# Kernel optimization log

Hardware: AMD Instinct MI355X
Metric: run time of the kernel (lower is better)

The kernel has to match this reference:

```python
import jax, jax.numpy as jnp
import numpy as np

B, N, FD, D, HF, WF = 4, 6, 256, 128, 64, 120
IMG_H, IMG_W = 480, 960
EPS_LN = 1e-5


def bilinear_sample(fmap, pts):
    """fmap: (B,C,H,W); pts: (B,P,2) xy pixel coords. Returns (B,P,C) values
    (zeros padding, align_corners=True convention) and (B,P) in-bounds mask."""
    Bc, C, H, W = fmap.shape
    flat = fmap.reshape(Bc, C, H * W)
    x, y = pts[..., 0], pts[..., 1]
    x0, y0 = jnp.floor(x), jnp.floor(y)
    out = jnp.zeros((Bc, pts.shape[1], C), fmap.dtype)
    for dx in (0.0, 1.0):
        for dy in (0.0, 1.0):
            cx, cy = x0 + dx, y0 + dy
            wgt = (1.0 - jnp.abs(x - cx)) * (1.0 - jnp.abs(y - cy))
            inb = (cx >= 0) & (cx <= W - 1) & (cy >= 0) & (cy <= H - 1)
            idx = (jnp.clip(cy, 0, H - 1) * W + jnp.clip(cx, 0, W - 1)).astype(jnp.int32)
            g = jnp.take_along_axis(flat, idx[:, None, :], axis=2)  # (B,C,P)
            out = out + (g * (wgt * inb)[:, None, :]).transpose(0, 2, 1)
    valid = (x >= 0) & (x <= W - 1) & (y >= 0) & (y <= H - 1)
    return out, valid


def _l2norm(x, axis):
    n = jnp.sqrt(jnp.sum(x * x, axis=axis, keepdims=True))
    return x / jnp.maximum(n, 1e-12)


def _ln(x, g, b):
    mu = jnp.mean(x, axis=-1, keepdims=True)
    var = jnp.mean((x - mu) ** 2, axis=-1, keepdims=True)
    return (x - mu) / jnp.sqrt(var + EPS_LN) * g + b


def setup_inputs() -> dict:
    key = jax.random.key(0)
    ks = jax.random.split(key, 12)
    rng = np.random.RandomState(0)
    feature = jax.random.normal(ks[0], (B, N, FD, HF, WF), jnp.float32)
    # realistic intrinsics (same K family for src/tar so homographies land in-frame)
    K = np.zeros((B, N, 3, 3), np.float32)
    K[..., 0, 0] = IMG_W * 0.8 * (1 + 0.01 * rng.randn(B, N))
    K[..., 1, 1] = IMG_W * 0.8 * (1 + 0.01 * rng.randn(B, N))
    K[..., 0, 2] = IMG_W / 2
    K[..., 1, 2] = IMG_H / 2
    K[..., 2, 2] = 1.0
    I_tar_inv = np.linalg.inv(K[:, 0]).astype(np.float32)  # (B,3,3)
    # extrinsics: near-identity rotation + small translation
    E = np.tile(np.eye(4, dtype=np.float32), (B, N, 1, 1))
    w = 0.02 * rng.randn(B, N, 3).astype(np.float32)
    skew = np.zeros((B, N, 3, 3), np.float32)
    skew[..., 0, 1], skew[..., 0, 2] = -w[..., 2], w[..., 1]
    skew[..., 1, 0], skew[..., 1, 2] = w[..., 2], -w[..., 0]
    skew[..., 2, 0], skew[..., 2, 1] = -w[..., 1], w[..., 0]
    E[..., :3, :3] = np.eye(3, dtype=np.float32) + skew
    E[..., :3, 3] = 0.1 * rng.randn(B, N, 3).astype(np.float32)
    nv = np.tile(np.array([0.0, -1.0, 0.0], np.float32), (B, 1, 1))
    nv += 0.01 * rng.randn(B, 1, 3).astype(np.float32)
    nv /= np.linalg.norm(nv, axis=-1, keepdims=True)
    sc_in, sc_hid = 1.0 / np.sqrt(FD), 1.0 / np.sqrt(D)
    return {
        "feature": feature,
        "I_src": jnp.asarray(K),
        "I_tar_inv": jnp.asarray(I_tar_inv),
        "E": jnp.asarray(E),
        "dis": jnp.float32(1.5),
        "norm_vec": jnp.asarray(nv),
        "bn_gamma": jnp.ones((FD,), jnp.float32),
        "bn_beta": jnp.zeros((FD,), jnp.float32),
        "bn_mean": jnp.zeros((FD,), jnp.float32),
        "bn_var": jnp.ones((FD,), jnp.float32),
        "conv_w": jax.random.normal(ks[1], (D, FD), jnp.float32) * sc_in,
        "ln1_g": jnp.ones((D,), jnp.float32),
        "ln1_b": jnp.zeros((D,), jnp.float32),
        "mlp_w1": jax.random.normal(ks[2], (D, 2 * D), jnp.float32) * sc_hid,
        "mlp_b1": jnp.zeros((2 * D,), jnp.float32),
        "mlp_w2": jax.random.normal(ks[3], (2 * D, D), jnp.float32) * sc_hid,
        "mlp_b2": jnp.zeros((D,), jnp.float32),
        "ln2_g": jnp.ones((D,), jnp.float32),
        "ln2_b": jnp.zeros((D,), jnp.float32),
    }


def reference(feature, I_src, I_tar_inv, E, dis, norm_vec, bn_gamma, bn_beta,
              bn_mean, bn_var, conv_w, ln1_g, ln1_b, mlp_w1, mlp_b1, mlp_w2,
              mlp_b2, ln2_g, ln2_b):
    b, n, fd, h, w = feature.shape
    d = conv_w.shape[0]
    P = h * w
    # feature_linear: BN (inference stats) + ReLU + 1x1 conv (no bias)
    f = (feature - bn_mean[:, None, None]) / jnp.sqrt(bn_var[:, None, None] + 1e-5)
    f = f * bn_gamma[:, None, None] + bn_beta[:, None, None]
    f = jax.nn.relu(f)
    val = jnp.einsum('of,bnfhw->bnohw', conv_w, f)  # (b,n,d,h,w)
    # homography of normalized grid scaled to image pixels
    xs = jnp.linspace(0.0, 1.0, w)
    ys = jnp.linspace(0.0, 1.0, h)
    X, Y = jnp.meshgrid(xs, ys)  # (h,w), xy indexing
    pix = jnp.stack([X.ravel() * IMG_W, Y.ravel() * IMG_H, jnp.ones(P)], 0)  # (3,P)
    R = E[..., :3, :3]
    T = E[..., :3, 3:]
    Hm = I_src @ (R - (T @ norm_vec[:, None]) / dis) @ I_tar_inv[:, None]  # (b,n,3,3)
    homo = jnp.einsum('bnij,jp->bnip', Hm, pix.astype(Hm.dtype))
    uv = homo[:, :, :2] / homo[:, :, 2:3]
    uv = uv / jnp.array([[IMG_W], [IMG_H]], uv.dtype)  # (b,n,2,P) in ~[0,1]
    # HomoGuideAttention
    pts = (uv * jnp.array([[w], [h]], uv.dtype)).transpose(0, 1, 3, 2).reshape(b * n, P, 2)
    sampled, valid = bilinear_sample(val.reshape(b * n, d, h, w), pts)  # (bn,P,d),(bn,P)
    keyv = _l2norm(sampled, axis=2).reshape(b, n, P, d)
    query = val[:, 0]  # (b,d,h,w)
    q = _l2norm(query.reshape(b, d, P), axis=1)
    dot = jnp.einsum('bdp,bnpd->bnp', q, keyv)
    dot = dot * valid.reshape(b, n, P).astype(dot.dtype)
    att = jax.nn.softmax(dot, axis=1)
    z = jnp.einsum('bnp,bnpd->bpd', att, sampled.reshape(b, n, P, d))
    z = z.transpose(0, 2, 1).reshape(b, d, h, w) + query
    z = z.reshape(b, d, P).transpose(0, 2, 1)  # (b,P,d)
    z = _ln(z, ln1_g, ln1_b)
    hmid = jax.nn.gelu(z @ mlp_w1 + mlp_b1, approximate=False)
    z = z + (hmid @ mlp_w2 + mlp_b2)
    z = _ln(z, ln2_g, ln2_b)
    return z.transpose(0, 2, 1).reshape(b, d, h, w)
```

## Files before the change

### kernel.cpp

```cpp
#include <hip/hip_runtime.h>
#include <hip/hip_bf16.h>
#include <math.h>

#define B_ 4
#define N_ 6
#define FD_ 256
#define D_ 128
#define HF_ 64
#define WF_ 120
#define P_ (HF_*WF_)

typedef __attribute__((ext_vector_type(8))) short short8;
typedef __attribute__((ext_vector_type(4))) float floatx4;
typedef __attribute__((ext_vector_type(4))) unsigned int uint4e;

__device__ inline float gred_sum(float v) {
  v += __shfl_xor(v, 1); v += __shfl_xor(v, 2);
  v += __shfl_xor(v, 4); v += __shfl_xor(v, 8);
  return v;
}

__device__ inline float gred32(float v) {
  v += __shfl_xor(v, 1); v += __shfl_xor(v, 2);
  v += __shfl_xor(v, 4); v += __shfl_xor(v, 8);
  v += __shfl_xor(v, 16);
  return v;
}

__device__ inline unsigned short f2bf(float f) {
  unsigned int u = __builtin_bit_cast(unsigned int, f);
  u += 0x7fffu + ((u >> 16) & 1u);
  return (unsigned short)(u >> 16);
}
__device__ inline float bf2f(unsigned short h) {
  return __builtin_bit_cast(float, ((unsigned int)h) << 16);
}
__device__ inline void bfu2(unsigned int u, float& lo, float& hi) {
  lo = __builtin_bit_cast(float, u << 16);
  hi = __builtin_bit_cast(float, u & 0xffff0000u);
}

__device__ inline void lds_barrier() {
  asm volatile("s_waitcnt lgkmcnt(0)\n\ts_barrier" ::: "memory");
}

__global__ void prep_kernel(const float* __restrict__ I_src, const float* __restrict__ I_tar_inv,
                            const float* __restrict__ E, const float* __restrict__ dis,
                            const float* __restrict__ norm_vec,
                            const float* __restrict__ bn_gamma, const float* __restrict__ bn_beta,
                            const float* __restrict__ bn_mean, const float* __restrict__ bn_var,
                            float* __restrict__ bnscale, float* __restrict__ bnbias,
                            float* __restrict__ Hm) {
  int t = threadIdx.x;
  if (t < FD_) {
    float s = bn_gamma[t] * rsqrtf(bn_var[t] + 1e-5f);
    bnscale[t] = s;
    bnbias[t] = bn_beta[t] - bn_mean[t] * s;
  }
  if (t < B_*N_) {
    int b = t / N_;
    const float* e = E + t*16;
    const float* nv = norm_vec + b*3;
    float inv_dis = 1.0f / dis[0];
    float M[9];
    #pragma unroll
    for (int r = 0; r < 3; r++)
      #pragma unroll
      for (int c = 0; c < 3; c++)
        M[r*3+c] = e[r*4+c] - e[r*4+3]*nv[c]*inv_dis;
    const float* Is = I_src + t*9;
    float A[9];
    #pragma unroll
    for (int r = 0; r < 3; r++)
      #pragma unroll
      for (int c = 0; c < 3; c++)
        A[r*3+c] = Is[r*3+0]*M[0*3+c] + Is[r*3+1]*M[1*3+c] + Is[r*3+2]*M[2*3+c];
    const float* It = I_tar_inv + b*9;
    #pragma unroll
    for (int r = 0; r < 3; r++)
      #pragma unroll
      for (int c = 0; c < 3; c++)
        Hm[t*9 + r*3+c] = A[r*3+0]*It[0*3+c] + A[r*3+1]*It[1*3+c] + A[r*3+2]*It[2*3+c];
  }
}

__global__ void uv_kernel(const float* __restrict__ Hm, float2* __restrict__ uvbuf) {
  int t = blockIdx.x * 256 + threadIdx.x;
  int p  = t % P_;
  int bn = t / P_;
  int py = p / WF_, px = p - py*WF_;
  float pixx = (float)px * (960.f/119.f);
  float pixy = (float)py * (480.f/63.f);
  const float* H = Hm + bn*9;
  float hx = H[0]*pixx + H[1]*pixy + H[2];
  float hy = H[3]*pixx + H[4]*pixy + H[5];
  float hz = H[6]*pixx + H[7]*pixy + H[8];
  float sx = (hx/hz) * ((float)WF_/960.f);
  float sy = (hy/hz) * ((float)HF_/480.f);
  uvbuf[t] = make_float2(sx, sy);
}

__global__ void swizzle_w_kernel(const float* __restrict__ conv_w, unsigned short* __restrict__ wswz) {
  int t = blockIdx.x * 256 + threadIdx.x;
  int j    =  t        & 7;
  int lane = (t >> 3)  & 63;
  int dt   = (t >> 9)  & 7;
  int kc   =  t >> 12;
  int d = dt*16 + (lane & 15);
  int k = kc*32 + (lane >> 4)*8 + j;
  wswz[t] = f2bf(conv_w[d*FD_ + k]);
}

__global__ void swizzle_mlp_kernel(const float* __restrict__ w1, const float* __restrict__ w2,
                                   unsigned short* __restrict__ w1s, unsigned short* __restrict__ w2s) {
  int t = blockIdx.x * 256 + threadIdx.x;
  if (t < 32768) {
    int j    =  t        & 7;
    int lane = (t >> 3)  & 63;
    int dt   = (t >> 9)  & 15;
    int kc   =  t >> 13;
    int n = dt*16 + (lane & 15);
    int k = kc*32 + (lane >> 4)*8 + j;
    w1s[t] = f2bf(w1[k*256 + n]);
  } else {
    int u = t - 32768;
    int j    =  u        & 7;
    int lane = (u >> 3)  & 63;
    int dt   = (u >> 9)  & 7;
    int kc   =  u >> 12;
    int n = dt*16 + (lane & 15);
    int k = kc*32 + (lane >> 4)*8 + j;
    w2s[u] = f2bf(w2[k*128 + n]);
  }
}

#define AST_ 36
__global__ __launch_bounds__(256) void conv_kernel(const float* __restrict__ feature,
    const unsigned short* __restrict__ wswz, const float* __restrict__ bnscale,
    const float* __restrict__ bnbias, unsigned short* __restrict__ val) {
  __shared__ __align__(16) char csm[19968];
  unsigned short* apadA = (unsigned short*)csm;
  unsigned short* apadB = (unsigned short*)(csm + 4608);
  unsigned short* ytile = (unsigned short*)csm;
  float* sbn = (float*)(csm + 17408);

  int tid = threadIdx.x;
  sbn[tid] = bnscale[tid]; sbn[256+tid] = bnbias[tid];

  int bn = blockIdx.y;
  int p0 = blockIdx.x * 64;
  const float* fbase2 = feature + (size_t)bn*FD_*P_ + p0;

  int K0 = tid >> 4;
  int sp = (tid & 15) * 4;

  int ln = tid & 63, wv = tid >> 6;
  int m = ln & 15, q = ln >> 4;
  int row = wv*16 + m;

  float4 va[2], vb[2];
  {
    const float* fb0 = fbase2 + (size_t)(2*K0)*P_ + sp;
    va[0] = *(const float4*)fb0; vb[0] = *(const float4*)(fb0 + P_);
    const float* fb1 = fbase2 + (size_t)(32 + 2*K0)*P_ + sp;
    va[1] = *(const float4*)fb1; vb[1] = *(const float4*)(fb1 + P_);
  }
  __syncthreads();

  floatx4 acc[8];
  #pragma unroll
  for (int dt = 0; dt < 8; dt++) acc[dt] = (floatx4){0.f,0.f,0.f,0.f};

  {
    int k0 = 0;
    float s0 = sbn[k0+2*K0],   b0 = sbn[256+k0+2*K0];
    float s1 = sbn[k0+2*K0+1], b1 = sbn[256+k0+2*K0+1];
    float a0[4] = {va[0].x, va[0].y, va[0].z, va[0].w};
    float a1[4] = {vb[0].x, vb[0].y, vb[0].z, vb[0].w};
    #pragma unroll
    for (int i = 0; i < 4; i++) {
      unsigned int w = (unsigned int)f2bf(fmaxf(a0[i]*s0+b0, 0.f))
                     | ((unsigned int)f2bf(fmaxf(a1[i]*s1+b1, 0.f)) << 16);
      *(unsigned int*)&apadA[(sp+i)*AST_ + 2*K0] = w;
    }
  }

  #pragma unroll
  for (int kc = 0; kc < 8; kc++) {
    lds_barrier();
    if (kc + 2 < 8) {
      const float* fb = fbase2 + (size_t)((kc+2)*32 + 2*K0)*P_ + sp;
      va[kc&1] = *(const float4*)fb;
      vb[kc&1] = *(const float4*)(fb + P_);
    }
    if (kc + 1 < 8) {
      int s = (kc+1)&1;
      int k0 = (kc+1)*32;
      unsigned short* ap = ((kc+1)&1) ? apadB : apadA;
      float s0 = sbn[k0+2*K0],   b0 = sbn[256+k0+2*K0];
      float s1 = sbn[k0+2*K0+1], b1 = sbn[256+k0+2*K0+1];
      float a0[4] = {va[s].x, va[s].y, va[s].z, va[s].w};
      float a1[4] = {vb[s].x, vb[s].y, vb[s].z, vb[s].w};
      #pragma unroll
      for (int i = 0; i < 4; i++) {
        unsigned int w = (unsigned int)f2bf(fmaxf(a0[i]*s0+b0, 0.f))
                       | ((unsigned int)f2bf(fmaxf(a1[i]*s1+b1, 0.f)) << 16);
        *(unsigned int*)&ap[(sp+i)*AST_ + 2*K0] = w;
      }
    }
    unsigned short* rp = (kc&1) ? apadB : apadA;
    uint2 u0 = *(const uint2*)&rp[row*AST_ + q*8];
    uint2 u1 = *(const uint2*)&rp[row*AST_ + q*8 + 4];
    uint4e ua = {u0.x, u0.y, u1.x, u1.y};
    short8 af = __builtin_bit_cast(short8, ua);
    #pragma unroll
    for (int dt = 0; dt < 8; dt++) {
      short8 bfg = *(const short8*)(wswz + (((size_t)kc*8 + dt)*64 + ln)*8);
      acc[dt] = __builtin_amdgcn_mfma_f32_16x16x32_bf16(af, bfg, acc[dt], 0, 0, 0);
    }
  }
  __syncthreads();

  #pragma unroll
  for (int dt = 0; dt < 8; dt++)
    #pragma unroll
    for (int r = 0; r < 4; r++)
      ytile[(wv*16 + q*4 + r)*136 + dt*16 + m] = f2bf(acc[dt][r]);
  __syncthreads();
  #pragma unroll
  for (int i = 0; i < 4; i++) {
    int idx = tid + i*256;
    int pp = idx >> 4, ch = idx & 15;
    uint4 v = *(const uint4*)&ytile[pp*136 + ch*8];
    *(uint4*)(val + ((size_t)bn*P_ + p0 + pp)*D_ + ch*8) = v;
  }
}

__global__ __launch_bounds__(256, 4) void att_kernel(const unsigned short* __restrict__ val,
    const float2* __restrict__ uvbuf, const float* __restrict__ ln1_g,
    const float* __restrict__ ln1_b, unsigned short* __restrict__ zbuf) {
  int b = blockIdx.y;
  int bx = blockIdx.x;
  int tile = (bx & 7) * 120 + (bx >> 3);
  int p0 = tile * 8;
  int tid = threadIdx.x;
  int ln = tid & 63, wv = tid >> 6;
  int grp = ln >> 5, c = ln & 31;
  int p = p0 + wv*2 + grp;

  float g1[4], be1[4];
  *(float4*)&g1[0]  = *(const float4*)(ln1_g + c*4);
  *(float4*)&be1[0] = *(const float4*)(ln1_b + c*4);

  uint2 qu = *(const uint2*)(val + ((size_t)(b*N_)*P_ + p)*D_ + c*4);
  float qv[4];
  bfu2(qu.x, qv[0], qv[1]); bfu2(qu.y, qv[2], qv[3]);
  float qp = 0.f;
  #pragma unroll
  for (int i = 0; i < 4; i++) qp += qv[i]*qv[i];
  float qinv = 1.f / fmaxf(sqrtf(gred32(qp)), 1e-12f);

  float dotv[N_];
  float sv[N_][4];
  #pragma unroll
  for (int np = 0; np < 3; np++) {
    uint2 g[2][4]; float wm[2][4]; bool vld[2];
    #pragma unroll
    for (int t = 0; t < 2; t++) {
      int n = np*2 + t;
      float2 uv = uvbuf[((size_t)(b*N_ + n))*P_ + p];
      float sx = uv.x, sy = uv.y;
      float x0f = floorf(sx), y0f = floorf(sy);
      float fx = sx - x0f, fy = sy - y0f;
      int x0 = (int)x0f, y0 = (int)y0f;
      const unsigned short* base = val + ((size_t)(b*N_+n)*P_)*D_ + c*4;
      #pragma unroll
      for (int k = 0; k < 4; k++) {
        int dx = k & 1, dy = k >> 1;
        int cx = x0 + dx, cy = y0 + dy;
        bool inb = (cx >= 0) && (cx <= WF_-1) && (cy >= 0) && (cy <= HF_-1);
        int icx = min(max(cx,0),WF_-1), icy = min(max(cy,0),HF_-1);
        wm[t][k] = inb ? (dx ? fx : 1.f-fx) * (dy ? fy : 1.f-fy) : 0.f;
        g[t][k] = *(const uint2*)(base + (size_t)(icy*WF_ + icx)*D_);
      }
      vld[t] = (sx >= 0.f) && (sx <= (float)(WF_-1)) && (sy >= 0.f) && (sy <= (float)(HF_-1));
    }
    #pragma unroll
    for (int t = 0; t < 2; t++) {
      int n = np*2 + t;
      float acc[4];
      #pragma unroll
      for (int i = 0; i < 4; i++) acc[i] = 0.f;
      #pragma unroll
      for (int k = 0; k < 4; k++) {
        float gg[4];
        bfu2(g[t][k].x, gg[0], gg[1]); bfu2(g[t][k].y, gg[2], gg[3]);
        float w = wm[t][k];
        #pragma unroll
        for (int i = 0; i < 4; i++) acc[i] += gg[i]*w;
      }
      float ssp = 0.f, qsp = 0.f;
      #pragma unroll
      for (int i = 0; i < 4; i++) { ssp += acc[i]*acc[i]; qsp += qv[i]*acc[i]; }
      float ss = gred32(ssp);
      float qs = gred32(qsp);
      float dn = qs * qinv / fmaxf(sqrtf(ss), 1e-12f);
      dotv[n] = vld[t] ? dn : 0.f;
      #pragma unroll
      for (int i = 0; i < 4; i++) sv[n][i] = acc[i];
    }
  }
  float mx = dotv[0];
  #pragma unroll
  for (int n = 1; n < N_; n++) mx = fmaxf(mx, dotv[n]);
  float e[N_]; float den = 0.f;
  #pragma unroll
  for (int n = 0; n < N_; n++) { e[n] = expf(dotv[n]-mx); den += e[n]; }
  float rden = 1.f/den;
  float z[4];
  #pragma unroll
  for (int i = 0; i < 4; i++) z[i] = qv[i];
  #pragma unroll
  for (int n = 0; n < N_; n++) {
    float a = e[n]*rden;
    #pragma unroll
    for (int i = 0; i < 4; i++) z[i] += a*sv[n][i];
  }
  float sp = 0.f;
  #pragma unroll
  for (int i = 0; i < 4; i++) sp += z[i];
  float mu = gred32(sp) * (1.f/128.f);
  float vp = 0.f;
  #pragma unroll
  for (int i = 0; i < 4; i++) { float d0 = z[i]-mu; vp += d0*d0; }
  float rs = rsqrtf(gred32(vp) * (1.f/128.f) + 1e-5f);
  unsigned int ow[2];
  #pragma unroll
  for (int i = 0; i < 2; i++) {
    float o0 = (z[2*i]-mu)*rs*g1[2*i] + be1[2*i];
    float o1 = (z[2*i+1]-mu)*rs*g1[2*i+1] + be1[2*i+1];
    ow[i] = (unsigned int)f2bf(o0) | ((unsigned int)f2bf(o1) << 16);
  }
  *(uint2*)(zbuf + ((size_t)b*P_ + p)*D_ + c*4) = make_uint2(ow[0], ow[1]);
}

__global__ __launch_bounds__(256) void mlp_kernel(const unsigned short* __restrict__ zbuf,
    const unsigned short* __restrict__ w1s, const float* __restrict__ b1,
    const unsigned short* __restrict__ w2s, const float* __restrict__ b2,
    const float* __restrict__ ln2_g, const float* __restrict__ ln2_b,
    float* __restrict__ out) {
  __shared__ __align__(16) char smem[26112];
  unsigned short* zt = (unsigned short*)smem;
  unsigned short* ht = (unsigned short*)(smem + 8704);
  float* lnp = (float*)(smem + 25600);
  float* yt = (float*)smem;

  int tid = threadIdx.x;
  int b = blockIdx.y;
  int p0 = blockIdx.x * 32;
  int ln = tid & 63, wv = tid >> 6;
  int m = ln & 15, q = ln >> 4;
  int h = wv >> 1, ch2 = wv & 1;

  #pragma unroll
  for (int i = 0; i < 2; i++) {
    int idx = tid + i*256;
    int pp = idx >> 4, ch = idx & 15;
    *(uint4*)&zt[pp*136 + ch*8] = *(const uint4*)(zbuf + ((size_t)b*P_ + p0 + pp)*D_ + ch*8);
  }
  __syncthreads();

  floatx4 a1[8];
  #pragma unroll
  for (int j = 0; j < 8; j++) a1[j] = (floatx4){0.f,0.f,0.f,0.f};
  #pragma unroll
  for (int kc = 0; kc < 4; kc++) {
    short8 af = *(const short8*)&zt[(h*16+m)*136 + kc*32 + q*8];
    #pragma unroll
    for (int j = 0; j < 8; j++) {
      int dt = ch2*8 + j;
      short8 bfg = *(const short8*)(w1s + (((size_t)kc*16 + dt)*64 + ln)*8);
      a1[j] = __builtin_amdgcn_mfma_f32_16x16x32_bf16(af, bfg, a1[j], 0, 0, 0);
    }
  }
  #pragma unroll
  for (int j = 0; j < 8; j++) {
    int dt = ch2*8 + j;
    float bb = b1[dt*16 + m];
    #pragma unroll
    for (int r = 0; r < 4; r++) {
      float x = a1[j][r] + bb;
      float hv = 0.5f*x*(1.f + erff(x*0.70710678118654752f));
      ht[(h*16 + q*4 + r)*264 + dt*16 + m] = f2bf(hv);
    }
  }
  __syncthreads();

  floatx4 a2[4];
  #pragma unroll
  for (int j = 0; j < 4; j++) a2[j] = (floatx4){0.f,0.f,0.f,0.f};
  #pragma unroll
  for (int kc = 0; kc < 8; kc++) {
    short8 af = *(const short8*)&ht[(h*16+m)*264 + kc*32 + q*8];
    #pragma unroll
    for (int j = 0; j < 4; j++) {
      int dt = ch2*4 + j;
      short8 bfg = *(const short8*)(w2s + (((size_t)kc*8 + dt)*64 + ln)*8);
      a2[j] = __builtin_amdgcn_mfma_f32_16x16x32_bf16(af, bfg, a2[j], 0, 0, 0);
    }
  }
  float y[4][4];
  #pragma unroll
  for (int j = 0; j < 4; j++) {
    int dt = ch2*4 + j;
    float bb = b2[dt*16 + m];
    #pragma unroll
    for (int r = 0; r < 4; r++) {
      int pp = h*16 + q*4 + r;
      y[j][r] = a2[j][r] + bb + bf2f(zt[pp*136 + dt*16 + m]);
    }
  }
  #pragma unroll
  for (int r = 0; r < 4; r++) {
    float sp = 0.f, sq = 0.f;
    #pragma unroll
    for (int j = 0; j < 4; j++) { sp += y[j][r]; sq += y[j][r]*y[j][r]; }
    sp = gred_sum(sp); sq = gred_sum(sq);
    if (m == 0) {
      int pl = h*16 + q*4 + r;
      lnp[(ch2*32 + pl)*2 + 0] = sp;
      lnp[(ch2*32 + pl)*2 + 1] = sq;
    }
  }
  __syncthreads();
  float mu_[4], rs_[4];
  #pragma unroll
  for (int r = 0; r < 4; r++) {
    int pl = h*16 + q*4 + r;
    float sum = lnp[pl*2]     + lnp[(32+pl)*2];
    float ssq = lnp[pl*2 + 1] + lnp[(32+pl)*2 + 1];
    float mu = sum * (1.f/128.f);
    float var = fmaxf(ssq * (1.f/128.f) - mu*mu, 0.f);
    mu_[r] = mu; rs_[r] = rsqrtf(var + 1e-5f);
  }
  float gg[4], be[4];
  #pragma unroll
  for (int j = 0; j < 4; j++) {
    int d = (ch2*4 + j)*16 + m;
    gg[j] = ln2_g[d]; be[j] = ln2_b[d];
  }
  #pragma unroll
  for (int j = 0; j < 4; j++)
    #pragma unroll
    for (int r = 0; r < 4; r++)
      y[j][r] = (y[j][r] - mu_[r])*rs_[r]*gg[j] + be[j];
  __syncthreads();
  #pragma unroll
  for (int j = 0; j < 4; j++)
    #pragma unroll
    for (int r = 0; r < 4; r++)
      yt[((ch2*4 + j)*16 + m)*34 + h*16 + q*4 + r] = y[j][r];
  __syncthreads();

  #pragma unroll
  for (int i = 0; i < 8; i++) {
    int idx = tid + i*256;
    int d = idx >> 4, pu = idx & 15;
    *(float2*)(out + ((size_t)(b*D_ + d))*P_ + p0 + pu*2) = *(float2*)&yt[d*34 + pu*2];
  }
}

extern "C" void kernel_launch(void* const* d_in, const int* in_sizes, int n_in,
                              void* d_out, int out_size, void* d_ws, size_t ws_size,
                              hipStream_t stream) {
  (void)in_sizes; (void)n_in; (void)out_size; (void)ws_size;
  const float* feature   = (const float*)d_in[0];
  const float* I_src     = (const float*)d_in[1];
  const float* I_tar_inv = (const float*)d_in[2];
  const float* E         = (const float*)d_in[3];
  const float* dis       = (const float*)d_in[4];
  const float* norm_vec  = (const float*)d_in[5];
  const float* bn_gamma  = (const float*)d_in[6];
  const float* bn_beta   = (const float*)d_in[7];
  const float* bn_mean   = (const float*)d_in[8];
  const float* bn_var    = (const float*)d_in[9];
  const float* conv_w    = (const float*)d_in[10];
  const float* ln1_g     = (const float*)d_in[11];
  const float* ln1_b     = (const float*)d_in[12];
  const float* mlp_w1    = (const float*)d_in[13];
  const float* mlp_b1    = (const float*)d_in[14];
  const float* mlp_w2    = (const float*)d_in[15];
  const float* mlp_b2    = (const float*)d_in[16];
  const float* ln2_g     = (const float*)d_in[17];
  const float* ln2_b     = (const float*)d_in[18];
  float* out = (float*)d_out;

  char* ws = (char*)d_ws;
  float* bnscale       = (float*)(ws + 0);
  float* bnbias        = (float*)(ws + 1024);
  float* Hm            = (float*)(ws + 2048);
  unsigned short* wswz = (unsigned short*)(ws + 4096);
  unsigned short* w1s  = (unsigned short*)(ws + 69632);
  unsigned short* w2s  = (unsigned short*)(ws + 135168);
  float2* uvbuf        = (float2*)(ws + 200704);
  unsigned short* val  = (unsigned short*)(ws + 1675264);
  unsigned short* zbuf = (unsigned short*)(ws + 1675264 + 47185920ULL);

  hipLaunchKernelGGL(prep_kernel, dim3(1), dim3(256), 0, stream,
                     I_src, I_tar_inv, E, dis, norm_vec,
                     bn_gamma, bn_beta, bn_mean, bn_var, bnscale, bnbias, Hm);
  hipLaunchKernelGGL(uv_kernel, dim3(720), dim3(256), 0, stream, Hm, uvbuf);
  hipLaunchKernelGGL(swizzle_w_kernel, dim3(128), dim3(256), 0, stream, conv_w, wswz);
  hipLaunchKernelGGL(swizzle_mlp_kernel, dim3(256), dim3(256), 0, stream,
                     mlp_w1, mlp_w2, w1s, w2s);
  hipLaunchKernelGGL(conv_kernel, dim3(120, 24), dim3(256), 0, stream,
                     feature, wswz, bnscale, bnbias, val);
  hipLaunchKernelGGL(att_kernel, dim3(960, 4), dim3(256), 0, stream,
                     val, uvbuf, ln1_g, ln1_b, zbuf);
  hipLaunchKernelGGL(mlp_kernel, dim3(240, 4), dim3(256), 0, stream,
                     zbuf, w1s, mlp_b1, w2s, mlp_b2, ln2_g, ln2_b, out);
}
```

Measured before the change: 359.3 us.

## Fuse attention into MLP kernel and merge setup kernels into one launch

Merges the attention stage into the MLP kernel so the layer-normed attention output goes straight into shared memory, with no round trip through a global bf16 buffer. Each block now covers 32 pixels over four attention passes. The prep, uv and weight-swizzle kernels become one setup kernel, with the homography recomputed per thread, and the BN scale/bias computation moves into the conv kernel prologue. This removes three launches and the zbuf write and read, but it lowers attention-stage parallelism and may raise register pressure in the fused kernel.

```diff
diff --git a/kernel.cpp b/kernel.cpp
--- a/kernel.cpp
+++ b/kernel.cpp
@@ -44,22 +44,22 @@
   asm volatile("s_waitcnt lgkmcnt(0)\n\ts_barrier" ::: "memory");
 }
 
-__global__ void prep_kernel(const float* __restrict__ I_src, const float* __restrict__ I_tar_inv,
-                            const float* __restrict__ E, const float* __restrict__ dis,
-                            const float* __restrict__ norm_vec,
-                            const float* __restrict__ bn_gamma, const float* __restrict__ bn_beta,
-                            const float* __restrict__ bn_mean, const float* __restrict__ bn_var,
-                            float* __restrict__ bnscale, float* __restrict__ bnbias,
-                            float* __restrict__ Hm) {
-  int t = threadIdx.x;
-  if (t < FD_) {
-    float s = bn_gamma[t] * rsqrtf(bn_var[t] + 1e-5f);
-    bnscale[t] = s;
-    bnbias[t] = bn_beta[t] - bn_mean[t] * s;
-  }
-  if (t < B_*N_) {
-    int b = t / N_;
-    const float* e = E + t*16;
+__global__ __launch_bounds__(256) void setup_kernel(
+    const float* __restrict__ I_src, const float* __restrict__ I_tar_inv,
+    const float* __restrict__ E, const float* __restrict__ dis,
+    const float* __restrict__ norm_vec,
+    const float* __restrict__ conv_w, const float* __restrict__ w1,
+    const float* __restrict__ w2,
+    float2* __restrict__ uvbuf, unsigned short* __restrict__ wswz,
+    unsigned short* __restrict__ w1s, unsigned short* __restrict__ w2s) {
+  int bx = blockIdx.x;
+  int tid = threadIdx.x;
+  if (bx < 720) {
+    int t = bx*256 + tid;
+    int p  = t % P_;
+    int bn = t / P_;
+    int b  = bn / N_;
+    const float* e  = E + bn*16;
     const float* nv = norm_vec + b*3;
     float inv_dis = 1.0f / dis[0];
     float M[9];
@@ -68,7 +68,7 @@
       #pragma unroll
       for (int c = 0; c < 3; c++)
         M[r*3+c] = e[r*4+c] - e[r*4+3]*nv[c]*inv_dis;
-    const float* Is = I_src + t*9;
+    const float* Is = I_src + bn*9;
     float A[9];
     #pragma unroll
     for (int r = 0; r < 3; r++)
@@ -76,68 +76,59 @@
       for (int c = 0; c < 3; c++)
         A[r*3+c] = Is[r*3+0]*M[0*3+c] + Is[r*3+1]*M[1*3+c] + Is[r*3+2]*M[2*3+c];
     const float* It = I_tar_inv + b*9;
+    float H[9];
     #pragma unroll
     for (int r = 0; r < 3; r++)
       #pragma unroll
       for (int c = 0; c < 3; c++)
-        Hm[t*9 + r*3+c] = A[r*3+0]*It[0*3+c] + A[r*3+1]*It[1*3+c] + A[r*3+2]*It[2*3+c];
-  }
-}
-
-__global__ void uv_kernel(const float* __restrict__ Hm, float2* __restrict__ uvbuf) {
-  int t = blockIdx.x * 256 + threadIdx.x;
-  int p  = t % P_;
-  int bn = t / P_;
-  int py = p / WF_, px = p - py*WF_;
-  float pixx = (float)px * (960.f/119.f);
-  float pixy = (float)py * (480.f/63.f);
-  const float* H = Hm + bn*9;
-  float hx = H[0]*pixx + H[1]*pixy + H[2];
-  float hy = H[3]*pixx + H[4]*pixy + H[5];
-  float hz = H[6]*pixx + H[7]*pixy + H[8];
-  float sx = (hx/hz) * ((float)WF_/960.f);
-  float sy = (hy/hz) * ((float)HF_/480.f);
-  uvbuf[t] = make_float2(sx, sy);
-}
-
-__global__ void swizzle_w_kernel(const float* __restrict__ conv_w, unsigned short* __restrict__ wswz) {
-  int t = blockIdx.x * 256 + threadIdx.x;
-  int j    =  t        & 7;
-  int lane = (t >> 3)  & 63;
-  int dt   = (t >> 9)  & 7;
-  int kc   =  t >> 12;
-  int d = dt*16 + (lane & 15);
-  int k = kc*32 + (lane >> 4)*8 + j;
-  wswz[t] = f2bf(conv_w[d*FD_ + k]);
-}
-
-__global__ void swizzle_mlp_kernel(const float* __restrict__ w1, const float* __restrict__ w2,
-                                   unsigned short* __restrict__ w1s, unsigned short* __restrict__ w2s) {
-  int t = blockIdx.x * 256 + threadIdx.x;
-  if (t < 32768) {
+        H[r*3+c] = A[r*3+0]*It[0*3+c] + A[r*3+1]*It[1*3+c] + A[r*3+2]*It[2*3+c];
+    int py = p / WF_, px = p - py*WF_;
+    float pixx = (float)px * (960.f/119.f);
+    float pixy = (float)py * (480.f/63.f);
+    float hx = H[0]*pixx + H[1]*pixy + H[2];
+    float hy = H[3]*pixx + H[4]*pixy + H[5];
+    float hz = H[6]*pixx + H[7]*pixy + H[8];
+    float sx = (hx/hz) * ((float)WF_/960.f);
+    float sy = (hy/hz) * ((float)HF_/480.f);
+    uvbuf[t] = make_float2(sx, sy);
+  } else if (bx < 848) {
+    int t = (bx-720)*256 + tid;
     int j    =  t        & 7;
     int lane = (t >> 3)  & 63;
-    int dt   = (t >> 9)  & 15;
-    int kc   =  t >> 13;
-    int n = dt*16 + (lane & 15);
+    int dt   = (t >> 9)  & 7;
+    int kc   =  t >> 12;
+    int d = dt*16 + (lane & 15);
     int k = kc*32 + (lane >> 4)*8 + j;
-    w1s[t] = f2bf(w1[k*256 + n]);
+    wswz[t] = f2bf(conv_w[d*FD_ + k]);
   } else {
-    int u = t - 32768;
-    int j    =  u        & 7;
-    int lane = (u >> 3)  & 63;
-    int dt   = (u >> 9)  & 7;
-    int kc   =  u >> 12;
-    int n = dt*16 + (lane & 15);
-    int k = kc*32 + (lane >> 4)*8 + j;
-    w2s[u] = f2bf(w2[k*128 + n]);
+    int t = (bx-848)*256 + tid;
+    if (t < 32768) {
+      int j    =  t        & 7;
+      int lane = (t >> 3)  & 63;
+      int dt   = (t >> 9)  & 15;
+      int kc   =  t >> 13;
+      int n = dt*16 + (lane & 15);
+      int k = kc*32 + (lane >> 4)*8 + j;
+      w1s[t] = f2bf(w1[k*256 + n]);
+    } else {
+      int u = t - 32768;
+      int j    =  u        & 7;
+      int lane = (u >> 3)  & 63;
+      int dt   = (u >> 9)  & 7;
+      int kc   =  u >> 12;
+      int n = dt*16 + (lane & 15);
+      int k = kc*32 + (lane >> 4)*8 + j;
+      w2s[u] = f2bf(w2[k*128 + n]);
+    }
   }
 }
 
 #define AST_ 36
 __global__ __launch_bounds__(256) void conv_kernel(const float* __restrict__ feature,
-    const unsigned short* __restrict__ wswz, const float* __restrict__ bnscale,
-    const float* __restrict__ bnbias, unsigned short* __restrict__ val) {
+    const unsigned short* __restrict__ wswz,
+    const float* __restrict__ bn_gamma, const float* __restrict__ bn_beta,
+    const float* __restrict__ bn_mean, const float* __restrict__ bn_var,
+    unsigned short* __restrict__ val) {
   __shared__ __align__(16) char csm[19968];
   unsigned short* apadA = (unsigned short*)csm;
   unsigned short* apadB = (unsigned short*)(csm + 4608);
@@ -145,7 +136,11 @@
   float* sbn = (float*)(csm + 17408);
 
   int tid = threadIdx.x;
-  sbn[tid] = bnscale[tid]; sbn[256+tid] = bnbias[tid];
+  {
+    float s = bn_gamma[tid] * rsqrtf(bn_var[tid] + 1e-5f);
+    sbn[tid] = s;
+    sbn[256+tid] = bn_beta[tid] - bn_mean[tid] * s;
+  }
 
   int bn = blockIdx.y;
   int p0 = blockIdx.x * 64;
@@ -236,115 +231,9 @@
   }
 }
 
-__global__ __launch_bounds__(256, 4) void att_kernel(const unsigned short* __restrict__ val,
-    const float2* __restrict__ uvbuf, const float* __restrict__ ln1_g,
-    const float* __restrict__ ln1_b, unsigned short* __restrict__ zbuf) {
-  int b = blockIdx.y;
-  int bx = blockIdx.x;
-  int tile = (bx & 7) * 120 + (bx >> 3);
-  int p0 = tile * 8;
-  int tid = threadIdx.x;
-  int ln = tid & 63, wv = tid >> 6;
-  int grp = ln >> 5, c = ln & 31;
-  int p = p0 + wv*2 + grp;
-
-  float g1[4], be1[4];
-  *(float4*)&g1[0]  = *(const float4*)(ln1_g + c*4);
-  *(float4*)&be1[0] = *(const float4*)(ln1_b + c*4);
-
-  uint2 qu = *(const uint2*)(val + ((size_t)(b*N_)*P_ + p)*D_ + c*4);
-  float qv[4];
-  bfu2(qu.x, qv[0], qv[1]); bfu2(qu.y, qv[2], qv[3]);
-  float qp = 0.f;
-  #pragma unroll
-  for (int i = 0; i < 4; i++) qp += qv[i]*qv[i];
-  float qinv = 1.f / fmaxf(sqrtf(gred32(qp)), 1e-12f);
-
-  float dotv[N_];
-  float sv[N_][4];
-  #pragma unroll
-  for (int np = 0; np < 3; np++) {
-    uint2 g[2][4]; float wm[2][4]; bool vld[2];
-    #pragma unroll
-    for (int t = 0; t < 2; t++) {
-      int n = np*2 + t;
-      float2 uv = uvbuf[((size_t)(b*N_ + n))*P_ + p];
-      float sx = uv.x, sy = uv.y;
-      float x0f = floorf(sx), y0f = floorf(sy);
-      float fx = sx - x0f, fy = sy - y0f;
-      int x0 = (int)x0f, y0 = (int)y0f;
-      const unsigned short* base = val + ((size_t)(b*N_+n)*P_)*D_ + c*4;
-      #pragma unroll
-      for (int k = 0; k < 4; k++) {
-        int dx = k & 1, dy = k >> 1;
-        int cx = x0 + dx, cy = y0 + dy;
-        bool inb = (cx >= 0) && (cx <= WF_-1) && (cy >= 0) && (cy <= HF_-1);
-        int icx = min(max(cx,0),WF_-1), icy = min(max(cy,0),HF_-1);
-        wm[t][k] = inb ? (dx ? fx : 1.f-fx) * (dy ? fy : 1.f-fy) : 0.f;
-        g[t][k] = *(const uint2*)(base + (size_t)(icy*WF_ + icx)*D_);
-      }
-      vld[t] = (sx >= 0.f) && (sx <= (float)(WF_-1)) && (sy >= 0.f) && (sy <= (float)(HF_-1));
-    }
-    #pragma unroll
-    for (int t = 0; t < 2; t++) {
-      int n = np*2 + t;
-      float acc[4];
-      #pragma unroll
-      for (int i = 0; i < 4; i++) acc[i] = 0.f;
-      #pragma unroll
-      for (int k = 0; k < 4; k++) {
-        float gg[4];
-        bfu2(g[t][k].x, gg[0], gg[1]); bfu2(g[t][k].y, gg[2], gg[3]);
-        float w = wm[t][k];
-        #pragma unroll
-        for (int i = 0; i < 4; i++) acc[i] += gg[i]*w;
-      }
-      float ssp = 0.f, qsp = 0.f;
-      #pragma unroll
-      for (int i = 0; i < 4; i++) { ssp += acc[i]*acc[i]; qsp += qv[i]*acc[i]; }
-      float ss = gred32(ssp);
-      float qs = gred32(qsp);
-      float dn = qs * qinv / fmaxf(sqrtf(ss), 1e-12f);
-      dotv[n] = vld[t] ? dn : 0.f;
-      #pragma unroll
-      for (int i = 0; i < 4; i++) sv[n][i] = acc[i];
-    }
-  }
-  float mx = dotv[0];
-  #pragma unroll
-  for (int n = 1; n < N_; n++) mx = fmaxf(mx, dotv[n]);
-  float e[N_]; float den = 0.f;
-  #pragma unroll
-  for (int n = 0; n < N_; n++) { e[n] = expf(dotv[n]-mx); den += e[n]; }
-  float rden = 1.f/den;
-  float z[4];
-  #pragma unroll
-  for (int i = 0; i < 4; i++) z[i] = qv[i];
-  #pragma unroll
-  for (int n = 0; n < N_; n++) {
-    float a = e[n]*rden;
-    #pragma unroll
-    for (int i = 0; i < 4; i++) z[i] += a*sv[n][i];
-  }
-  float sp = 0.f;
-  #pragma unroll
-  for (int i = 0; i < 4; i++) sp += z[i];
-  float mu = gred32(sp) * (1.f/128.f);
-  float vp = 0.f;
-  #pragma unroll
-  for (int i = 0; i < 4; i++) { float d0 = z[i]-mu; vp += d0*d0; }
-  float rs = rsqrtf(gred32(vp) * (1.f/128.f) + 1e-5f);
-  unsigned int ow[2];
-  #pragma unroll
-  for (int i = 0; i < 2; i++) {
-    float o0 = (z[2*i]-mu)*rs*g1[2*i] + be1[2*i];
-    float o1 = (z[2*i+1]-mu)*rs*g1[2*i+1] + be1[2*i+1];
-    ow[i] = (unsigned int)f2bf(o0) | ((unsigned int)f2bf(o1) << 16);
-  }
-  *(uint2*)(zbuf + ((size_t)b*P_ + p)*D_ + c*4) = make_uint2(ow[0], ow[1]);
-}
-
-__global__ __launch_bounds__(256) void mlp_kernel(const unsigned short* __restrict__ zbuf,
+__global__ __launch_bounds__(256, 4) void attmlp_kernel(
+    const unsigned short* __restrict__ val, const float2* __restrict__ uvbuf,
+    const float* __restrict__ ln1_g, const float* __restrict__ ln1_b,
     const unsigned short* __restrict__ w1s, const float* __restrict__ b1,
     const unsigned short* __restrict__ w2s, const float* __restrict__ b2,
     const float* __restrict__ ln2_g, const float* __restrict__ ln2_b,
@@ -357,18 +246,117 @@
 
   int tid = threadIdx.x;
   int b = blockIdx.y;
-  int p0 = blockIdx.x * 32;
+  int bx = blockIdx.x;
+  int tile = (bx & 7) * 30 + (bx >> 3);
+  int p0 = tile * 32;
   int ln = tid & 63, wv = tid >> 6;
+
+  {
+    int grp = ln >> 5, c = ln & 31;
+    float g1[4], be1[4];
+    *(float4*)&g1[0]  = *(const float4*)(ln1_g + c*4);
+    *(float4*)&be1[0] = *(const float4*)(ln1_b + c*4);
+
+    for (int pass = 0; pass < 4; pass++) {
+      int pl = pass*8 + wv*2 + grp;
+      int p = p0 + pl;
+
+      uint2 qu = *(const uint2*)(val + ((size_t)(b*N_)*P_ + p)*D_ + c*4);
+      float qv[4];
+      bfu2(qu.x, qv[0], qv[1]); bfu2(qu.y, qv[2], qv[3]);
+      float qp = 0.f;
+      #pragma unroll
+      for (int i = 0; i < 4; i++) qp += qv[i]*qv[i];
+      float qinv = 1.f / fmaxf(sqrtf(gred32(qp)), 1e-12f);
+
+      float dotv[N_];
+      float sv[N_][4];
+      #pragma unroll
+      for (int np = 0; np < 3; np++) {
+        uint2 g[2][4]; float wm[2][4]; bool vld[2];
+        #pragma unroll
+        for (int t = 0; t < 2; t++) {
+          int n = np*2 + t;
+          float2 uv = uvbuf[((size_t)(b*N_ + n))*P_ + p];
+          float sx = uv.x, sy = uv.y;
+          float x0f = floorf(sx), y0f = floorf(sy);
+          float fx = sx - x0f, fy = sy - y0f;
+          int x0 = (int)x0f, y0 = (int)y0f;
+          const unsigned short* base = val + ((size_t)(b*N_+n)*P_)*D_ + c*4;
+          #pragma unroll
+          for (int k = 0; k < 4; k++) {
+            int dx = k & 1, dy = k >> 1;
+            int cx = x0 + dx, cy = y0 + dy;
+            bool inb = (cx >= 0) && (cx <= WF_-1) && (cy >= 0) && (cy <= HF_-1);
+            int icx = min(max(cx,0),WF_-1), icy = min(max(cy,0),HF_-1);
+            wm[t][k] = inb ? (dx ? fx : 1.f-fx) * (dy ? fy : 1.f-fy) : 0.f;
+            g[t][k] = *(const uint2*)(base + (size_t)(icy*WF_ + icx)*D_);
+          }
+          vld[t] = (sx >= 0.f) && (sx <= (float)(WF_-1)) && (sy >= 0.f) && (sy <= (float)(HF_-1));
+        }
+        #pragma unroll
+        for (int t = 0; t < 2; t++) {
+          int n = np*2 + t;
+          float acc[4];
+          #pragma unroll
+          for (int i = 0; i < 4; i++) acc[i] = 0.f;
+          #pragma unroll
+          for (int k = 0; k < 4; k++) {
+            float gg[4];
+            bfu2(g[t][k].x, gg[0], gg[1]); bfu2(g[t][k].y, gg[2], gg[3]);
+            float w = wm[t][k];
+            #pragma unroll
+            for (int i = 0; i < 4; i++) acc[i] += gg[i]*w;
+          }
+          float ssp = 0.f, qsp = 0.f;
+          #pragma unroll
+          for (int i = 0; i < 4; i++) { ssp += acc[i]*acc[i]; qsp += qv[i]*acc[i]; }
+          float ss = gred32(ssp);
+          float qs = gred32(qsp);
+          float dn = qs * qinv / fmaxf(sqrtf(ss), 1e-12f);
+          dotv[n] = vld[t] ? dn : 0.f;
+          #pragma unroll
+          for (int i = 0; i < 4; i++) sv[n][i] = acc[i];
+        }
+      }
+      float mx = dotv[0];
+      #pragma unroll
+      for (int n = 1; n < N_; n++) mx = fmaxf(mx, dotv[n]);
+      float e[N_]; float den = 0.f;
+      #pragma unroll
+      for (int n = 0; n < N_; n++) { e[n] = expf(dotv[n]-mx); den += e[n]; }
+      float rden = 1.f/den;
+      float z[4];
+      #pragma unroll
+      for (int i = 0; i < 4; i++) z[i] = qv[i];
+      #pragma unroll
+      for (int n = 0; n < N_; n++) {
+        float a = e[n]*rden;
+        #pragma unroll
+        for (int i = 0; i < 4; i++) z[i] += a*sv[n][i];
+      }
+      float sp = 0.f;
+      #pragma unroll
+      for (int i = 0; i < 4; i++) sp += z[i];
+      float mu = gred32(sp) * (1.f/128.f);
+      float vp = 0.f;
+      #pragma unroll
+      for (int i = 0; i < 4; i++) { float d0 = z[i]-mu; vp += d0*d0; }
+      float rs = rsqrtf(gred32(vp) * (1.f/128.f) + 1e-5f);
+      unsigned int ow[2];
+      #pragma unroll
+      for (int i = 0; i < 2; i++) {
+        float o0 = (z[2*i]-mu)*rs*g1[2*i] + be1[2*i];
+        float o1 = (z[2*i+1]-mu)*rs*g1[2*i+1] + be1[2*i+1];
+        ow[i] = (unsigned int)f2bf(o0) | ((unsigned int)f2bf(o1) << 16);
+      }
+      *(uint2*)&zt[pl*136 + c*4] = make_uint2(ow[0], ow[1]);
+    }
+  }
+  __syncthreads();
+
   int m = ln & 15, q = ln >> 4;
   int h = wv >> 1, ch2 = wv & 1;
-
-  #pragma unroll
-  for (int i = 0; i < 2; i++) {
-    int idx = tid + i*256;
-    int pp = idx >> 4, ch = idx & 15;
-    *(uint4*)&zt[pp*136 + ch*8] = *(const uint4*)(zbuf + ((size_t)b*P_ + p0 + pp)*D_ + ch*8);
-  }
-  __syncthreads();
 
   floatx4 a1[8];
   #pragma unroll
@@ -496,27 +484,19 @@
   float* out = (float*)d_out;
 
   char* ws = (char*)d_ws;
-  float* bnscale       = (float*)(ws + 0);
-  float* bnbias        = (float*)(ws + 1024);
-  float* Hm            = (float*)(ws + 2048);
-  unsigned short* wswz = (unsigned short*)(ws + 4096);
-  unsigned short* w1s  = (unsigned short*)(ws + 69632);
-  unsigned short* w2s  = (unsigned short*)(ws + 135168);
-  float2* uvbuf        = (float2*)(ws + 200704);
-  unsigned short* val  = (unsigned short*)(ws + 1675264);
-  unsigned short* zbuf = (unsigned short*)(ws + 1675264 + 47185920ULL);
-
-  hipLaunchKernelGGL(prep_kernel, dim3(1), dim3(256), 0, stream,
+  unsigned short* wswz = (unsigned short*)(ws + 0);
+  unsigned short* w1s  = (unsigned short*)(ws + 65536);
+  unsigned short* w2s  = (unsigned short*)(ws + 131072);
+  float2* uvbuf        = (float2*)(ws + 196608);
+  unsigned short* val  = (unsigned short*)(ws + 1671168);
+
+  hipLaunchKernelGGL(setup_kernel, dim3(1104), dim3(256), 0, stream,
                      I_src, I_tar_inv, E, dis, norm_vec,
-                     bn_gamma, bn_beta, bn_mean, bn_var, bnscale, bnbias, Hm);
-  hipLaunchKernelGGL(uv_kernel, dim3(720), dim3(256), 0, stream, Hm, uvbuf);
-  hipLaunchKernelGGL(swizzle_w_kernel, dim3(128), dim3(256), 0, stream, conv_w, wswz);
-  hipLaunchKernelGGL(swizzle_mlp_kernel, dim3(256), dim3(256), 0, stream,
-                     mlp_w1, mlp_w2, w1s, w2s);
+                     conv_w, mlp_w1, mlp_w2,
+                     uvbuf, wswz, w1s, w2s);
   hipLaunchKernelGGL(conv_kernel, dim3(120, 24), dim3(256), 0, stream,
-                     feature, wswz, bnscale, bnbias, val);
-  hipLaunchKernelGGL(att_kernel, dim3(960, 4), dim3(256), 0, stream,
-                     val, uvbuf, ln1_g, ln1_b, zbuf);
-  hipLaunchKernelGGL(mlp_kernel, dim3(240, 4), dim3(256), 0, stream,
-                     zbuf, w1s, mlp_b1, w2s, mlp_b2, ln2_g, ln2_b, out);
-}
+                     feature, wswz, bn_gamma, bn_beta, bn_mean, bn_var, val);
+  hipLaunchKernelGGL(attmlp_kernel, dim3(240, 4), dim3(256), 0, stream,
+                     val, uvbuf, ln1_g, ln1_b,
+                     w1s, mlp_b1, w2s, mlp_b2, ln2_g, ln2_b, out);
+}
```

New measurement: 358.6 us. Within noise of the previous version (-0.2%).
